# Kernel tuning notes

Measured on AMD Instinct MI355X. Metric: run time of the kernel, lower is better.

## Reference

```python
import jax, jax.numpy as jnp
import numpy as np

L, H, DIN, B, T = 2, 512, 512, 64, 1024


def _run_layer(seq, h0, Wih, Whh, bih, bhh):
    """GRU layer over time. seq: [T,B,Din], h0: [B,H]. Returns ([T,B,H], [B,H])."""
    gx = jnp.einsum('tbd,gd->tbg', seq, Wih) + bih  # [T,B,3H] input proj, batched

    def step(h, gx_t):
        gh = h @ Whh.T + bhh  # [B,3H]
        xr, xz, xn = jnp.split(gx_t, 3, axis=-1)
        hr, hz, hn = jnp.split(gh, 3, axis=-1)
        r = jax.nn.sigmoid(xr + hr)
        z = jax.nn.sigmoid(xz + hz)
        n = jnp.tanh(xn + r * hn)
        h_new = (1.0 - z) * n + z * h
        return h_new, h_new

    hT, ys = jax.lax.scan(step, h0, gx)
    return ys, hT


def setup_inputs() -> dict:
    key = jax.random.key(0)
    ks = jax.random.split(key, 10)
    s = 1.0 / np.sqrt(H)
    u = lambda k, shp: jax.random.uniform(k, shp, jnp.float32, -s, s)
    return {
        'x': jax.random.normal(ks[0], (B, T, DIN), jnp.float32),
        'encoder_h': jax.random.normal(ks[1], (L, B, 2 * H), jnp.float32),
        'Wih_f': u(ks[2], (L, 3 * H, DIN)),
        'Whh_f': u(ks[3], (L, 3 * H, H)),
        'bih_f': u(ks[4], (L, 3 * H)),
        'bhh_f': u(ks[5], (L, 3 * H)),
        'Wih_b': u(ks[6], (L, 3 * H, DIN)),
        'Whh_b': u(ks[7], (L, 3 * H, H)),
        'bih_b': u(ks[8], (L, 3 * H)),
        'bhh_b': u(ks[9], (L, 3 * H)),
    }


def reference(x, encoder_h, Wih_f, Whh_f, bih_f, bhh_f, Wih_b, Whh_b, bih_b, bhh_b):
    num_layers = Wih_f.shape[0]
    hidden = Whh_f.shape[-1]
    seq_f = jnp.transpose(x, (1, 0, 2))          # [T,B,D]
    seq_b = seq_f[::-1]                           # time-reversed input
    h_f, h_b = [], []
    for j in range(num_layers):
        seq_f, hf = _run_layer(seq_f, encoder_h[j, :, :hidden], Wih_f[j], Whh_f[j], bih_f[j], bhh_f[j])
        seq_b, hb = _run_layer(seq_b, encoder_h[j, :, hidden:], Wih_b[j], Whh_b[j], bih_b[j], bhh_b[j])
        h_f.append(hf)
        h_b.append(hb)
    out_f = jnp.transpose(seq_f, (1, 0, 2))       # [B,T,H]
    out_b = jnp.transpose(seq_b[::-1], (1, 0, 2))  # flip back to original time order
    out = jnp.concatenate([out_f, out_b], axis=2)  # [B,T,2H]
    h = jnp.concatenate([jnp.stack(h_f, 0), jnp.stack(h_b, 0)], axis=2)  # [L,B,2H]
    return out, h
```

## Files before the change

kernel.cpp:

```cpp
#include <hip/hip_runtime.h>
#include <hip/hip_bf16.h>
#include <cstdint>
#include <cstddef>

#define T_LEN 1024
#define B_SZ  64
#define H_DIM 512
#define D_IN  512
#define YSLOTS 16

#define GROUP 16

typedef __attribute__((ext_vector_type(8))) short short8;
typedef __attribute__((ext_vector_type(4))) float f32x4;
typedef unsigned long long ull;

#define OFF_WHH 0
#define OFF_X   98304
#define OFF_H   114688
#define OFF_D   131072
#define SMEM_BYTES 143360

__device__ __forceinline__ int swz(int row, int b) {
  return b ^ ((row & 7) << 4);
}

__device__ __forceinline__ unsigned short f2bf(float f) {
  unsigned u = __float_as_uint(f);
  return (unsigned short)((u + 0x7FFFu + ((u >> 16) & 1u)) >> 16);
}

__device__ __forceinline__ short8 pack8(float4 a, float4 b) {
  short8 v;
  v[0] = (short)f2bf(a.x); v[1] = (short)f2bf(a.y);
  v[2] = (short)f2bf(a.z); v[3] = (short)f2bf(a.w);
  v[4] = (short)f2bf(b.x); v[5] = (short)f2bf(b.y);
  v[6] = (short)f2bf(b.z); v[7] = (short)f2bf(b.w);
  return v;
}

__device__ __forceinline__ unsigned cvtpk(float lo, float hi) {
  unsigned r;
  asm("v_cvt_pk_bf16_f32 %0, %1, %2" : "=v"(r) : "v"(lo), "v"(hi));
  return r;
}
__device__ __forceinline__ short8 cvtpk8(float4 a, float4 b) {
  union { unsigned u[4]; short8 s; } cv;
  cv.u[0] = cvtpk(a.x, a.y); cv.u[1] = cvtpk(a.z, a.w);
  cv.u[2] = cvtpk(b.x, b.y); cv.u[3] = cvtpk(b.z, b.w);
  return cv.s;
}

__device__ __forceinline__ float sigm(float x) { return 1.0f / (1.0f + __expf(-x)); }
__device__ __forceinline__ float fast_tanh(float x) { return 1.0f - 2.0f / (__expf(2.0f * x) + 1.0f); }

__global__ __launch_bounds__(256, 1)
void gru_pipe(const float* __restrict__ x,
              const float* __restrict__ enc,
              const float* __restrict__ WihF, const float* __restrict__ WhhF,
              const float* __restrict__ bihF, const float* __restrict__ bhhF,
              const float* __restrict__ WihB, const float* __restrict__ WhhB,
              const float* __restrict__ bihB, const float* __restrict__ bhhB,
              float* __restrict__ dout,
              unsigned* __restrict__ flags,
              unsigned short* __restrict__ hbuf,
              unsigned short* __restrict__ yring)
{
  __shared__ alignas(16) char smem[SMEM_BYTES];

  const int bid   = blockIdx.x;
  const int layer = bid >> 7;
  const int lbid  = bid & 127;
  const int grp   = lbid & 7;
  const int dir   = grp >> 2;
  const int bg    = grp & 3;
  const int cg    = lbid >> 3;
  const int tid   = threadIdx.x;
  const int wv    = tid >> 6;
  const int tb    = tid >> 4;
  const int tc    = tid & 15;
  const int lane  = tid & 63;
  const int frow  = lane & 15;
  const int q     = lane >> 4;
  const int hc0   = cg * 32;
  const int c0    = hc0 + tc;
  const int c1    = c0 + 16;
  const int brow  = bg * 16 + tb;
  const int dircol = dir * H_DIM;
  const int gw = wv & 1, cw = wv >> 1, kh = wv & 1;

  const float* Wih = (dir ? WihB : WihF) + (size_t)layer * 3 * H_DIM * D_IN;
  const float* Whh = (dir ? WhhB : WhhF) + (size_t)layer * 3 * H_DIM * H_DIM;
  const float* bih = (dir ? bihB : bihF) + (size_t)layer * 3 * H_DIM;
  const float* bhh = (dir ? bhhB : bhhF) + (size_t)layer * 3 * H_DIM;

  unsigned* fl  = flags + (layer * 8 + grp) * 64;
  unsigned* fl0 = flags + grp * 64;
  unsigned* fl1 = flags + (8 + grp) * 64;

  #pragma unroll
  for (int g = 0; g < 3; ++g) {
    #pragma unroll
    for (int ch = 0; ch < 2; ++ch) {
      const float* s = Whh + (size_t)(g * H_DIM + hc0 + ch * 16 + tb) * H_DIM + tc * 32;
      char* r = smem + OFF_WHH + (g * 2 + ch) * 16384 + tb * 1024;
      #pragma unroll
      for (int u = 0; u < 4; ++u) {
        float4 a = ((const float4*)s)[u * 2];
        float4 b = ((const float4*)s)[u * 2 + 1];
        *(short8*)(r + swz(tb, tc * 64 + u * 16)) = pack8(a, b);
      }
    }
  }

  short8 wfM[16], wfN[8];
  {
    const float* pm = Wih + (size_t)(gw * H_DIM + hc0 + cw * 16 + frow) * D_IN;
    #pragma unroll
    for (int kc = 0; kc < 16; ++kc)
      wfM[kc] = cvtpk8(*(const float4*)(pm + kc * 32 + q * 8),
                       *(const float4*)(pm + kc * 32 + q * 8 + 4));
    const float* pn = Wih + (size_t)(2 * H_DIM + hc0 + cw * 16 + frow) * D_IN;
    #pragma unroll
    for (int j = 0; j < 8; ++j) {
      const int kc = kh * 8 + j;
      wfN[j] = cvtpk8(*(const float4*)(pn + kc * 32 + q * 8),
                      *(const float4*)(pn + kc * 32 + q * 8 + 4));
    }
  }

  const float b_r0  = bih[c0] + bhh[c0];
  const float b_z0  = bih[H_DIM + c0] + bhh[H_DIM + c0];
  const float b_xn0 = bih[2 * H_DIM + c0];
  const float b_hn0 = bhh[2 * H_DIM + c0];
  const float b_r1  = bih[c1] + bhh[c1];
  const float b_z1  = bih[H_DIM + c1] + bhh[H_DIM + c1];
  const float b_xn1 = bih[2 * H_DIM + c1];
  const float b_hn1 = bhh[2 * H_DIM + c1];
  float h0 = enc[(size_t)layer * B_SZ * 2 * H_DIM + (size_t)brow * 2 * H_DIM + dircol + c0];
  float h1 = enc[(size_t)layer * B_SZ * 2 * H_DIM + (size_t)brow * 2 * H_DIM + dircol + c1];

  auto hbase = [&](int par) -> unsigned short* {
    return hbuf + (size_t)((((layer * 2 + par) * 2 + dir) * 4 + bg) * 16) * 512;
  };
  auto ybase = [&](int slot) -> unsigned short* {
    return yring + (size_t)(((slot * 2 + dir) * 4 + bg) * 16) * 512;
  };

  auto pub = [&](float v0, float v1, unsigned short* hrow, unsigned short* yrow) {
    unsigned a = f2bf(v0), b = f2bf(v1);
    unsigned a1 = __shfl_down(a, 1), a2 = __shfl_down(a, 2), a3 = __shfl_down(a, 3);
    unsigned b1 = __shfl_down(b, 1), b2 = __shfl_down(b, 2), b3 = __shfl_down(b, 3);
    if ((tc & 3) == 0) {
      ull pa = (ull)a | ((ull)a1 << 16) | ((ull)a2 << 32) | ((ull)a3 << 48);
      ull pb = (ull)b | ((ull)b1 << 16) | ((ull)b2 << 32) | ((ull)b3 << 48);
      __hip_atomic_store((ull*)(hrow + hc0 + tc),      pa, __ATOMIC_RELAXED, __HIP_MEMORY_SCOPE_AGENT);
      __hip_atomic_store((ull*)(hrow + hc0 + 16 + tc), pb, __ATOMIC_RELAXED, __HIP_MEMORY_SCOPE_AGENT);
      if (yrow) {
        __hip_atomic_store((ull*)(yrow + hc0 + tc),      pa, __ATOMIC_RELAXED, __HIP_MEMORY_SCOPE_AGENT);
        __hip_atomic_store((ull*)(yrow + hc0 + 16 + tc), pb, __ATOMIC_RELAXED, __HIP_MEMORY_SCOPE_AGENT);
      }
    }
  };

  auto spin16 = [&](unsigned* f, unsigned tgt) {
    if (tid < GROUP) {
      while (__hip_atomic_load(&f[tid], __ATOMIC_RELAXED, __HIP_MEMORY_SCOPE_AGENT) < tgt)
        __builtin_amdgcn_s_sleep(1);
    }
  };

  auto gatherRow = [&](const unsigned short* src, int ldsOff) {
    const ull* hb = (const ull*)(src + (size_t)tb * 512 + tc * 32);
    ull hv[8];
    #pragma unroll
    for (int u = 0; u < 8; ++u)
      hv[u] = __hip_atomic_load(hb + u, __ATOMIC_RELAXED, __HIP_MEMORY_SCOPE_AGENT);
    char* lh = smem + ldsOff + tb * 1024;
    #pragma unroll
    for (int u = 0; u < 4; ++u) {
      ull tmp[2] = {hv[2 * u], hv[2 * u + 1]};
      *(short8*)(lh + swz(tb, tc * 64 + u * 16)) = *(const short8*)tmp;
    }
  };

  auto stage_x = [&](int pos) {
    const float* xrow = x + ((size_t)brow * T_LEN + pos) * D_IN;
    const float4* s4 = (const float4*)(xrow + tc * 32);
    char* lx = smem + OFF_X + tb * 1024;
    #pragma unroll
    for (int u = 0; u < 4; ++u) {
      float4 a = s4[u * 2];
      float4 b = s4[u * 2 + 1];
      *(short8*)(lx + swz(tb, tc * 64 + u * 16)) = pack8(a, b);
    }
  };

  auto xpart = [&](f32x4& aM, f32x4& aXN) {
    char* xr = smem + OFF_X + frow * 1024;
    #pragma unroll
    for (int kc = 0; kc < 16; ++kc) {
      short8 a = *(const short8*)(xr + swz(frow, kc * 64 + q * 16));
      aM = __builtin_amdgcn_mfma_f32_16x16x32_bf16(a, wfM[kc], aM, 0, 0, 0);
    }
    #pragma unroll
    for (int j = 0; j < 8; ++j) {
      const int kc = kh * 8 + j;
      short8 a = *(const short8*)(xr + swz(frow, kc * 64 + q * 16));
      aXN = __builtin_amdgcn_mfma_f32_16x16x32_bf16(a, wfN[j], aXN, 0, 0, 0);
    }
  };
  auto hpart = [&](f32x4& aM, f32x4& aHN) {
    char* hr = smem + OFF_H + frow * 1024;
    char* wm = smem + OFF_WHH + (gw * 2 + cw) * 16384 + frow * 1024;
    char* wn = smem + OFF_WHH + (4 + cw) * 16384 + frow * 1024;
    #pragma unroll
    for (int kc = 0; kc < 16; ++kc) {
      const int o = swz(frow, kc * 64 + q * 16);
      short8 a = *(const short8*)(hr + o);
      short8 b = *(const short8*)(wm + o);
      aM = __builtin_amdgcn_mfma_f32_16x16x32_bf16(a, b, aM, 0, 0, 0);
    }
    #pragma unroll
    for (int j = 0; j < 8; ++j) {
      const int kc = kh * 8 + j;
      const int o = swz(frow, kc * 64 + q * 16);
      short8 a = *(const short8*)(hr + o);
      short8 b = *(const short8*)(wn + o);
      aHN = __builtin_amdgcn_mfma_f32_16x16x32_bf16(a, b, aHN, 0, 0, 0);
    }
  };
  auto dwrite = [&](const f32x4& aM, const f32x4& aXN, const f32x4& aHN) {
    float* d0 = (float*)(smem + OFF_D + wv * 1024);
    float* d1 = (float*)(smem + OFF_D + 4096 + wv * 1024);
    float* d2 = (float*)(smem + OFF_D + 8192 + wv * 1024);
    #pragma unroll
    for (int r = 0; r < 4; ++r) {
      const int idx = (q * 4 + r) * 16 + ((frow + 4 * q) & 15);
      d0[idx] = aM[r]; d1[idx] = aXN[r]; d2[idx] = aHN[r];
    }
  };

  pub(h0, h1, hbase(0) + (size_t)tb * 512, nullptr);
  asm volatile("s_waitcnt vmcnt(0)" ::: "memory");
  __syncthreads();
  if (tid == 0)
    __hip_atomic_store(&fl[cg], 1u, __ATOMIC_RELAXED, __HIP_MEMORY_SCOPE_AGENT);

  f32x4 aM = {0.f,0.f,0.f,0.f}, aXN = {0.f,0.f,0.f,0.f};
  if (layer == 0) {
    stage_x(dir ? (T_LEN - 1) : 0);
    __syncthreads();
    xpart(aM, aXN);
  } else {
    spin16(fl0, 2u);
    __syncthreads();
    gatherRow(ybase(0), OFF_X);
    __syncthreads();
    xpart(aM, aXN);
  }

  for (int t = 0; t < T_LEN; ++t) {
    if (layer == 0 && t >= 16 && (t & 7) == 0)
      spin16(fl1, (unsigned)(t - 7));

    spin16(fl, (unsigned)(t + 1));
    __syncthreads();
    gatherRow(hbase(t & 1), OFF_H);
    __syncthreads();

    f32x4 aHN = {0.f,0.f,0.f,0.f};
    hpart(aM, aHN);
    dwrite(aM, aXN, aHN);
    __syncthreads();

    {
      const float* Df = (const float*)(smem + OFF_D);
      const int e = tb * 16 + ((tc + 4 * (tb >> 2)) & 15);
      const float r0 = sigm(Df[e] + b_r0);
      const float z0 = sigm(Df[256 + e] + b_z0);
      const float n0 = fast_tanh(Df[1024 + e] + Df[1280 + e] + b_xn0 +
                                 r0 * (Df[2048 + e] + Df[2304 + e] + b_hn0));
      h0 = (1.0f - z0) * n0 + z0 * h0;
      const float r1 = sigm(Df[512 + e] + b_r1);
      const float z1 = sigm(Df[768 + e] + b_z1);
      const float n1 = fast_tanh(Df[1536 + e] + Df[1792 + e] + b_xn1 +
                                 r1 * (Df[2560 + e] + Df[2816 + e] + b_hn1));
      h1 = (1.0f - z1) * n1 + z1 * h1;
    }

    const int torig = dir ? (T_LEN - 1 - t) : t;
    pub(h0, h1, hbase((t + 1) & 1) + (size_t)tb * 512,
        (layer == 0) ? (ybase(t & (YSLOTS - 1)) + (size_t)tb * 512) : nullptr);
    if (layer == 1) {
      dout[(size_t)brow * T_LEN * 2 * H_DIM + (size_t)torig * 2 * H_DIM + dircol + c0] = h0;
      dout[(size_t)brow * T_LEN * 2 * H_DIM + (size_t)torig * 2 * H_DIM + dircol + c1] = h1;
    }
    if (t == T_LEN - 1) {
      dout[(size_t)B_SZ * T_LEN * 2 * H_DIM +
           (size_t)(layer * B_SZ + brow) * 2 * H_DIM + dircol + c0] = h0;
      dout[(size_t)B_SZ * T_LEN * 2 * H_DIM +
           (size_t)(layer * B_SZ + brow) * 2 * H_DIM + dircol + c1] = h1;
    }
    asm volatile("s_waitcnt vmcnt(0)" ::: "memory");
    __syncthreads();
    if (tid == 0)
      __hip_atomic_store(&fl[cg], (unsigned)(t + 2), __ATOMIC_RELAXED, __HIP_MEMORY_SCOPE_AGENT);

    if (t + 1 < T_LEN) {
      if (layer == 0) {
        stage_x(dir ? (T_LEN - 2 - t) : (t + 1));
        __syncthreads();
      } else {
        spin16(fl0, (unsigned)(t + 3));
        __syncthreads();
        gatherRow(ybase((t + 1) & (YSLOTS - 1)), OFF_X);
        __syncthreads();
      }
      aM[0]=0.f;  aM[1]=0.f;  aM[2]=0.f;  aM[3]=0.f;
      aXN[0]=0.f; aXN[1]=0.f; aXN[2]=0.f; aXN[3]=0.f;
      xpart(aM, aXN);
    }
  }
}

extern "C" void kernel_launch(void* const* d_in, const int* in_sizes, int n_in,
                              void* d_out, int out_size, void* d_ws, size_t ws_size,
                              hipStream_t stream) {
  (void)in_sizes; (void)n_in; (void)out_size; (void)ws_size;
  const float* x    = (const float*)d_in[0];
  const float* enc  = (const float*)d_in[1];
  const float* WihF = (const float*)d_in[2];
  const float* WhhF = (const float*)d_in[3];
  const float* bihF = (const float*)d_in[4];
  const float* bhhF = (const float*)d_in[5];
  const float* WihB = (const float*)d_in[6];
  const float* WhhB = (const float*)d_in[7];
  const float* bihB = (const float*)d_in[8];
  const float* bhhB = (const float*)d_in[9];
  float* out = (float*)d_out;

  unsigned* flags = (unsigned*)d_ws;
  unsigned short* hbuf  = (unsigned short*)((char*)d_ws + 4096);
  unsigned short* yring = (unsigned short*)((char*)d_ws + 4096 + 524288);
  hipMemsetAsync(d_ws, 0, 4096, stream);

  dim3 grid(256), block(256);
  gru_pipe<<<grid, block, 0, stream>>>(x, enc, WihF, WhhF, bihF, bhhF,
                                       WihB, WhhB, bihB, bhhB, out, flags, hbuf, yring);
}
```

Before: 5.130 ms.

## Prefetch next x during recurrence and merge flag waits and gathers per step

Layer 0 now issues global loads for the next timestep's x into registers at the top of each step and packs them into LDS after the MFMA h-part, instead of staging x after publishing h. Layer 1 gathers the next y row together with the current h in one combined gather. All flag spins are merged into a single polling loop. This removes two barriers and one serial wait per step on the critical recurrence path. It adds register pressure from the prefetched x and makes the h wait also depend on the y and backpressure flags.

```diff
diff --git a/kernel.cpp b/kernel.cpp
--- a/kernel.cpp
+++ b/kernel.cpp
@@ -163,13 +163,6 @@
     }
   };
 
-  auto spin16 = [&](unsigned* f, unsigned tgt) {
-    if (tid < GROUP) {
-      while (__hip_atomic_load(&f[tid], __ATOMIC_RELAXED, __HIP_MEMORY_SCOPE_AGENT) < tgt)
-        __builtin_amdgcn_s_sleep(1);
-    }
-  };
-
   auto gatherRow = [&](const unsigned short* src, int ldsOff) {
     const ull* hb = (const ull*)(src + (size_t)tb * 512 + tc * 32);
     ull hv[8];
@@ -183,16 +176,24 @@
       *(short8*)(lh + swz(tb, tc * 64 + u * 16)) = *(const short8*)tmp;
     }
   };
-
-  auto stage_x = [&](int pos) {
-    const float* xrow = x + ((size_t)brow * T_LEN + pos) * D_IN;
-    const float4* s4 = (const float4*)(xrow + tc * 32);
+  auto gatherRow2 = [&](const unsigned short* srcH, const unsigned short* srcY) {
+    const ull* hb = (const ull*)(srcH + (size_t)tb * 512 + tc * 32);
+    const ull* yb = (const ull*)(srcY + (size_t)tb * 512 + tc * 32);
+    ull hv[8], yv[8];
+    #pragma unroll
+    for (int u = 0; u < 8; ++u)
+      hv[u] = __hip_atomic_load(hb + u, __ATOMIC_RELAXED, __HIP_MEMORY_SCOPE_AGENT);
+    #pragma unroll
+    for (int u = 0; u < 8; ++u)
+      yv[u] = __hip_atomic_load(yb + u, __ATOMIC_RELAXED, __HIP_MEMORY_SCOPE_AGENT);
+    char* lh = smem + OFF_H + tb * 1024;
     char* lx = smem + OFF_X + tb * 1024;
     #pragma unroll
     for (int u = 0; u < 4; ++u) {
-      float4 a = s4[u * 2];
-      float4 b = s4[u * 2 + 1];
-      *(short8*)(lx + swz(tb, tc * 64 + u * 16)) = pack8(a, b);
+      ull t0[2] = {hv[2 * u], hv[2 * u + 1]};
+      *(short8*)(lh + swz(tb, tc * 64 + u * 16)) = *(const short8*)t0;
+      ull t1[2] = {yv[2 * u], yv[2 * u + 1]};
+      *(short8*)(lx + swz(tb, tc * 64 + u * 16)) = *(const short8*)t1;
     }
   };
 
@@ -249,11 +250,22 @@
 
   f32x4 aM = {0.f,0.f,0.f,0.f}, aXN = {0.f,0.f,0.f,0.f};
   if (layer == 0) {
-    stage_x(dir ? (T_LEN - 1) : 0);
+    const float* xrow = x + ((size_t)brow * T_LEN + (dir ? (T_LEN - 1) : 0)) * D_IN;
+    const float4* s4 = (const float4*)(xrow + tc * 32);
+    char* lx = smem + OFF_X + tb * 1024;
+    #pragma unroll
+    for (int u = 0; u < 4; ++u) {
+      float4 a = s4[u * 2];
+      float4 b = s4[u * 2 + 1];
+      *(short8*)(lx + swz(tb, tc * 64 + u * 16)) = pack8(a, b);
+    }
     __syncthreads();
     xpart(aM, aXN);
   } else {
-    spin16(fl0, 2u);
+    if (tid < GROUP) {
+      while (__hip_atomic_load(&fl0[tid], __ATOMIC_RELAXED, __HIP_MEMORY_SCOPE_AGENT) < 2u)
+        __builtin_amdgcn_s_sleep(1);
+    }
     __syncthreads();
     gatherRow(ybase(0), OFF_X);
     __syncthreads();
@@ -261,17 +273,49 @@
   }
 
   for (int t = 0; t < T_LEN; ++t) {
-    if (layer == 0 && t >= 16 && (t & 7) == 0)
-      spin16(fl1, (unsigned)(t - 7));
-
-    spin16(fl, (unsigned)(t + 1));
-    __syncthreads();
-    gatherRow(hbase(t & 1), OFF_H);
+    float4 xf[8];
+    if (layer == 0 && t + 1 < T_LEN) {
+      const float* xrow = x + ((size_t)brow * T_LEN + (dir ? (T_LEN - 2 - t) : (t + 1))) * D_IN;
+      const float4* s4 = (const float4*)(xrow + tc * 32);
+      #pragma unroll
+      for (int u = 0; u < 8; ++u) xf[u] = s4[u];
+    }
+
+    {
+      const bool needY  = (layer == 1) && (t + 1 < T_LEN);
+      const bool needBP = (layer == 0) && (t >= 16) && ((t & 7) == 0);
+      if (tid < GROUP) {
+        const unsigned tgtH  = (unsigned)(t + 1);
+        const unsigned tgtY  = (unsigned)(t + 3);
+        const unsigned tgtBP = (unsigned)(t - 7);
+        for (;;) {
+          bool ok = __hip_atomic_load(&fl[tid], __ATOMIC_RELAXED, __HIP_MEMORY_SCOPE_AGENT) >= tgtH;
+          if (needY)
+            ok &= __hip_atomic_load(&fl0[tid], __ATOMIC_RELAXED, __HIP_MEMORY_SCOPE_AGENT) >= tgtY;
+          if (needBP)
+            ok &= __hip_atomic_load(&fl1[tid], __ATOMIC_RELAXED, __HIP_MEMORY_SCOPE_AGENT) >= tgtBP;
+          if (ok) break;
+          __builtin_amdgcn_s_sleep(1);
+        }
+      }
+    }
+    __syncthreads();
+
+    if (layer == 1 && t + 1 < T_LEN)
+      gatherRow2(hbase(t & 1), ybase((t + 1) & (YSLOTS - 1)));
+    else
+      gatherRow(hbase(t & 1), OFF_H);
     __syncthreads();
 
     f32x4 aHN = {0.f,0.f,0.f,0.f};
     hpart(aM, aHN);
     dwrite(aM, aXN, aHN);
+    if (layer == 0 && t + 1 < T_LEN) {
+      char* lx = smem + OFF_X + tb * 1024;
+      #pragma unroll
+      for (int u = 0; u < 4; ++u)
+        *(short8*)(lx + swz(tb, tc * 64 + u * 16)) = pack8(xf[u * 2], xf[u * 2 + 1]);
+    }
     __syncthreads();
 
     {
@@ -308,15 +352,6 @@
       __hip_atomic_store(&fl[cg], (unsigned)(t + 2), __ATOMIC_RELAXED, __HIP_MEMORY_SCOPE_AGENT);
 
     if (t + 1 < T_LEN) {
-      if (layer == 0) {
-        stage_x(dir ? (T_LEN - 2 - t) : (t + 1));
-        __syncthreads();
-      } else {
-        spin16(fl0, (unsigned)(t + 3));
-        __syncthreads();
-        gatherRow(ybase((t + 1) & (YSLOTS - 1)), OFF_X);
-        __syncthreads();
-      }
       aM[0]=0.f;  aM[1]=0.f;  aM[2]=0.f;  aM[3]=0.f;
       aXN[0]=0.f; aXN[1]=0.f; aXN[2]=0.f; aXN[3]=0.f;
       xpart(aM, aXN);
```

New measurement: 5.246 ms. 1.02x slower.
